# Kernel optimization log

Hardware: AMD Instinct MI355X
Metric: run time of the kernel (lower is better)

The kernel has to match this reference:

```python
import jax, jax.numpy as jnp
import numpy as np

NUM_CAPSULE = 5
DIM_CAPSULE = 5
ROUTINGS = 4
EPS = 1e-7


def squash(t, axis=-1):
    sn = jnp.sum(t * t, axis=axis, keepdims=True)
    scale = sn / (1.0 + sn)
    return scale * t / jnp.sqrt(sn + EPS)


def setup_inputs() -> dict:
    key = jax.random.key(0)
    kx, kw = jax.random.split(key)
    B, I, F = 8192, 256, 80
    x = jax.random.normal(kx, (B, I, F), dtype=jnp.float32)
    # xavier_normal for Linear(80 -> 25): std = sqrt(2/(fan_in+fan_out))
    std = np.sqrt(2.0 / (F + NUM_CAPSULE * DIM_CAPSULE))
    W = jax.random.normal(kw, (NUM_CAPSULE * DIM_CAPSULE, F), dtype=jnp.float32) * std
    return {"x": x, "W": W}


def reference(x, W):
    B, I, _ = x.shape
    # u_hat_vecs: [B, I, N*D] -> [B, N, I, D]
    u_hat = jnp.einsum('bif,of->bio', x, W)
    u_hat = u_hat.reshape(B, I, NUM_CAPSULE, DIM_CAPSULE).transpose(0, 2, 1, 3)
    b = jnp.zeros((B, NUM_CAPSULE, I), dtype=u_hat.dtype)
    outputs = None
    for i in range(ROUTINGS):
        c = jax.nn.softmax(b, axis=1)                         # [B, N, I]
        outputs = squash(jnp.einsum('bni,bnid->bnd', c, u_hat))  # [B, N, D]
        if i < ROUTINGS - 1:
            b = b + jnp.einsum('bnd,bnid->bni', outputs, u_hat)
    return outputs
```

## Files before the change

### kernel.cpp

```cpp
#include <hip/hip_runtime.h>

#define NCAP 5
#define DCAP 5
#define NO 25
#define II 256
#define FF 80
#define NROUT 4
#define EPS 1e-7f
#define USTR 28

typedef _Float16 f16x8 __attribute__((ext_vector_type(8)));
typedef __fp16 fp16x2 __attribute__((ext_vector_type(2)));
typedef float f32x4 __attribute__((ext_vector_type(4)));

__device__ __forceinline__ f16x8 pack8(const float4 a, const float4 c) {
    union { fp16x2 p[4]; f16x8 v; } u;
    u.p[0] = __builtin_amdgcn_cvt_pkrtz(a.x, a.y);
    u.p[1] = __builtin_amdgcn_cvt_pkrtz(a.z, a.w);
    u.p[2] = __builtin_amdgcn_cvt_pkrtz(c.x, c.y);
    u.p[3] = __builtin_amdgcn_cvt_pkrtz(c.z, c.w);
    return u.v;
}

template<int CTRL>
__device__ __forceinline__ float dpp_add(float v) {
    int sw = __builtin_amdgcn_update_dpp(0, __float_as_int(v), CTRL, 0xF, 0xF, true);
    return v + __int_as_float(sw);
}
__device__ __forceinline__ float row16_sum(float v) {
    v = dpp_add<0xB1>(v);
    v = dpp_add<0x4E>(v);
    v = dpp_add<0x141>(v);
    v = dpp_add<0x140>(v);
    return v;
}

__global__ __launch_bounds__(256, 5)
void capsule_mfma(const float* __restrict__ x, const float* __restrict__ W,
                  float* __restrict__ out) {
    const int b    = blockIdx.x;
    const int t    = threadIdx.x;
    const int lane = t & 63;
    const int wv   = t >> 6;
    const int lr   = lane & 15;
    const int lg   = lane >> 4;

    __shared__ __align__(16) float u_lds[II * USTR];
    __shared__ __align__(16) float red[16 * 28];
    __shared__ __align__(16) float fsum[28];

    f16x8 Af[2][3];
#pragma unroll
    for (int ot = 0; ot < 2; ++ot)
#pragma unroll
        for (int ks = 0; ks < 3; ++ks) {
            const int row = ot * 16 + lr;
            const int k0  = ks * 32 + lg * 8;
            if (row < NO && k0 < FF) {
                const float4 a = *reinterpret_cast<const float4*>(&W[row * FF + k0]);
                const float4 c = *reinterpret_cast<const float4*>(&W[row * FF + k0 + 4]);
                Af[ot][ks] = pack8(a, c);
            } else {
                const f16x8 z = {};
                Af[ot][ks] = z;
            }
        }

    const int R0 = wv * 64;
    const float* __restrict__ xbase = x + (size_t)b * II * FF;

#pragma unroll
    for (int nt = 0; nt < 4; ++nt) {
        const int xrow = R0 + nt * 16 + lr;
        const float* __restrict__ xp = xbase + (size_t)xrow * FF;

        f16x8 Bf[3];
#pragma unroll
        for (int ks = 0; ks < 3; ++ks) {
            const int k0 = ks * 32 + lg * 8;
            if (k0 < FF) {
                const float4 a = *reinterpret_cast<const float4*>(xp + k0);
                const float4 c = *reinterpret_cast<const float4*>(xp + k0 + 4);
                Bf[ks] = pack8(a, c);
            } else {
                const f16x8 z = {};
                Bf[ks] = z;
            }
        }

        f32x4 acc0 = {0.f, 0.f, 0.f, 0.f};
        f32x4 acc1 = {0.f, 0.f, 0.f, 0.f};
#pragma unroll
        for (int ks = 0; ks < 3; ++ks) {
            acc0 = __builtin_amdgcn_mfma_f32_16x16x32_f16(Af[0][ks], Bf[ks], acc0, 0, 0, 0);
            acc1 = __builtin_amdgcn_mfma_f32_16x16x32_f16(Af[1][ks], Bf[ks], acc1, 0, 0, 0);
        }

        *reinterpret_cast<float4*>(&u_lds[xrow * USTR + lg * 4]) =
            *reinterpret_cast<float4*>(&acc0);
        if (lg < 3)
            *reinterpret_cast<float4*>(&u_lds[xrow * USTR + 16 + lg * 4]) =
                *reinterpret_cast<float4*>(&acc1);
    }

    float u[NO];
#pragma unroll
    for (int q = 0; q < 6; ++q) {
        const float4 v4 = *reinterpret_cast<const float4*>(&u_lds[t * USTR + q * 4]);
        u[q * 4] = v4.x; u[q * 4 + 1] = v4.y; u[q * 4 + 2] = v4.z; u[q * 4 + 3] = v4.w;
    }
    u[24] = u_lds[t * USTR + 24];

    float bb[NCAP];
#pragma unroll
    for (int n = 0; n < NCAP; ++n) bb[n] = 0.f;

#pragma unroll
    for (int r = 0; r < NROUT; ++r) {
        float c[NCAP];
        if (r == 0) {
#pragma unroll
            for (int n = 0; n < NCAP; ++n) c[n] = 0.2f;
        } else {
            float m = bb[0];
#pragma unroll
            for (int n = 1; n < NCAP; ++n) m = fmaxf(m, bb[n]);
            float ssum = 0.f;
#pragma unroll
            for (int n = 0; n < NCAP; ++n) { c[n] = __expf(bb[n] - m); ssum += c[n]; }
            const float inv = __frcp_rn(ssum);
#pragma unroll
            for (int n = 0; n < NCAP; ++n) c[n] *= inv;
        }

        float p[NO];
#pragma unroll
        for (int o = 0; o < NO; ++o) p[o] = row16_sum(c[o / DCAP] * u[o]);

        if ((t & 15) == 0) {
            float* rg = &red[(t >> 4) * 28];
#pragma unroll
            for (int q = 0; q < 6; ++q)
                *reinterpret_cast<float4*>(&rg[q * 4]) =
                    make_float4(p[q * 4], p[q * 4 + 1], p[q * 4 + 2], p[q * 4 + 3]);
            rg[24] = p[24];
        }
        __syncthreads();

        if (t < NO) {
            float ssum = 0.f;
#pragma unroll
            for (int g = 0; g < 16; ++g) ssum += red[g * 28 + t];
            fsum[t] = ssum;
        }
        __syncthreads();

        if (r < NROUT - 1) {
            float s[NO];
#pragma unroll
            for (int q = 0; q < 6; ++q) {
                const float4 sv = *reinterpret_cast<const float4*>(&fsum[q * 4]);
                s[q * 4 + 0] = sv.x; s[q * 4 + 1] = sv.y;
                s[q * 4 + 2] = sv.z; s[q * 4 + 3] = sv.w;
            }
            s[24] = fsum[24];
#pragma unroll
            for (int n = 0; n < NCAP; ++n) {
                float sn = 0.f, dot = 0.f;
#pragma unroll
                for (int d = 0; d < DCAP; ++d) {
                    const float sv = s[n * DCAP + d];
                    sn  = fmaf(sv, sv, sn);
                    dot = fmaf(sv, u[n * DCAP + d], dot);
                }
                const float scale = sn * __frsqrt_rn(sn + EPS) * __frcp_rn(1.f + sn);
                bb[n] += dot * scale;
            }
        } else {
            if (t < NO) {
                const int n0 = (t / DCAP) * DCAP;
                float sn = 0.f;
#pragma unroll
                for (int d = 0; d < DCAP; ++d) {
                    const float sv = fsum[n0 + d];
                    sn = fmaf(sv, sv, sn);
                }
                const float scale = sn * __frsqrt_rn(sn + EPS) * __frcp_rn(1.f + sn);
                out[(size_t)b * NO + t] = fsum[t] * scale;
            }
        }
    }
}

extern "C" void kernel_launch(void* const* d_in, const int* in_sizes, int n_in,
                              void* d_out, int out_size, void* d_ws, size_t ws_size,
                              hipStream_t stream) {
    const float* x = (const float*)d_in[0];
    const float* W = (const float*)d_in[1];
    float* out = (float*)d_out;
    (void)in_sizes; (void)n_in; (void)out_size; (void)d_ws; (void)ws_size;

    capsule_mfma<<<dim3(8192), dim3(256), 0, stream>>>(x, W, out);
}
```

Measured before the change: 125.5 us.

## Stage x tiles through LDS with double-buffered async global_load_lds

New measurement: 160.0 us. +27.5%, slower.

```diff
diff --git a/kernel.cpp b/kernel.cpp
--- a/kernel.cpp
+++ b/kernel.cpp
@@ -8,10 +8,14 @@
 #define NROUT 4
 #define EPS 1e-7f
 #define USTR 28
+#define CHUNK_F (16 * FF)
 
 typedef _Float16 f16x8 __attribute__((ext_vector_type(8)));
 typedef __fp16 fp16x2 __attribute__((ext_vector_type(2)));
 typedef float f32x4 __attribute__((ext_vector_type(4)));
+
+typedef __attribute__((address_space(1))) const void gvoid;
+typedef __attribute__((address_space(3))) void lvoid;
 
 __device__ __forceinline__ f16x8 pack8(const float4 a, const float4 c) {
     union { fp16x2 p[4]; f16x8 v; } u;
@@ -35,7 +39,7 @@
     return v;
 }
 
-__global__ __launch_bounds__(256, 5)
+__global__ __launch_bounds__(256, 2)
 void capsule_mfma(const float* __restrict__ x, const float* __restrict__ W,
                   float* __restrict__ out) {
     const int b    = blockIdx.x;
@@ -45,6 +49,7 @@
     const int lr   = lane & 15;
     const int lg   = lane >> 4;
 
+    __shared__ __align__(16) float stage[4][2][CHUNK_F];
     __shared__ __align__(16) float u_lds[II * USTR];
     __shared__ __align__(16) float red[16 * 28];
     __shared__ __align__(16) float fsum[28];
@@ -66,21 +71,41 @@
             }
         }
 
-    const int R0 = wv * 64;
-    const float* __restrict__ xbase = x + (size_t)b * II * FF;
+    const float* __restrict__ xw = x + ((size_t)b * II + wv * 64) * FF;
+
+    {
+        float* dst = &stage[wv][0][0];
+#pragma unroll
+        for (int c2 = 0; c2 < 5; ++c2)
+            __builtin_amdgcn_global_load_lds(
+                (gvoid*)(xw + c2 * 256 + lane * 4),
+                (lvoid*)(dst + c2 * 256), 16, 0, 0);
+    }
 
 #pragma unroll
     for (int nt = 0; nt < 4; ++nt) {
-        const int xrow = R0 + nt * 16 + lr;
-        const float* __restrict__ xp = xbase + (size_t)xrow * FF;
+        if (nt < 3) {
+            float* dst = &stage[wv][(nt + 1) & 1][0];
+            const float* src = xw + (nt + 1) * CHUNK_F;
+#pragma unroll
+            for (int c2 = 0; c2 < 5; ++c2)
+                __builtin_amdgcn_global_load_lds(
+                    (gvoid*)(src + c2 * 256 + lane * 4),
+                    (lvoid*)(dst + c2 * 256), 16, 0, 0);
+            asm volatile("s_waitcnt vmcnt(5)" ::: "memory");
+        } else {
+            asm volatile("s_waitcnt vmcnt(0)" ::: "memory");
+        }
+
+        const float* sb = &stage[wv][nt & 1][0];
 
         f16x8 Bf[3];
 #pragma unroll
         for (int ks = 0; ks < 3; ++ks) {
             const int k0 = ks * 32 + lg * 8;
             if (k0 < FF) {
-                const float4 a = *reinterpret_cast<const float4*>(xp + k0);
-                const float4 c = *reinterpret_cast<const float4*>(xp + k0 + 4);
+                const float4 a = *reinterpret_cast<const float4*>(&sb[lr * FF + k0]);
+                const float4 c = *reinterpret_cast<const float4*>(&sb[lr * FF + k0 + 4]);
                 Bf[ks] = pack8(a, c);
             } else {
                 const f16x8 z = {};
@@ -96,6 +121,7 @@
             acc1 = __builtin_amdgcn_mfma_f32_16x16x32_f16(Af[1][ks], Bf[ks], acc1, 0, 0, 0);
         }
 
+        const int xrow = wv * 64 + nt * 16 + lr;
         *reinterpret_cast<float4*>(&u_lds[xrow * USTR + lg * 4]) =
             *reinterpret_cast<float4*>(&acc0);
         if (lg < 3)
```

## Compute routing weighted sums with MFMA over transposed fp16 LDS tiles

Applied to the files above, without the earlier changes.

Result: slower. 179.8 us (+43.3%).

```diff
diff --git a/kernel.cpp b/kernel.cpp
--- a/kernel.cpp
+++ b/kernel.cpp
@@ -7,7 +7,8 @@
 #define FF 80
 #define NROUT 4
 #define EPS 1e-7f
-#define USTR 28
+#define TSTR 260
+#define CSTR 260
 
 typedef _Float16 f16x8 __attribute__((ext_vector_type(8)));
 typedef __fp16 fp16x2 __attribute__((ext_vector_type(2)));
@@ -22,19 +23,6 @@
     return u.v;
 }
 
-template<int CTRL>
-__device__ __forceinline__ float dpp_add(float v) {
-    int sw = __builtin_amdgcn_update_dpp(0, __float_as_int(v), CTRL, 0xF, 0xF, true);
-    return v + __int_as_float(sw);
-}
-__device__ __forceinline__ float row16_sum(float v) {
-    v = dpp_add<0xB1>(v);
-    v = dpp_add<0x4E>(v);
-    v = dpp_add<0x141>(v);
-    v = dpp_add<0x140>(v);
-    return v;
-}
-
 __global__ __launch_bounds__(256, 5)
 void capsule_mfma(const float* __restrict__ x, const float* __restrict__ W,
                   float* __restrict__ out) {
@@ -45,9 +33,9 @@
     const int lr   = lane & 15;
     const int lg   = lane >> 4;
 
-    __shared__ __align__(16) float u_lds[II * USTR];
-    __shared__ __align__(16) float red[16 * 28];
-    __shared__ __align__(16) float fsum[28];
+    __shared__ __align__(16) _Float16 uT[32 * TSTR];
+    __shared__ __align__(16) _Float16 cT[16 * CSTR];
+    __shared__ __align__(16) float s_lds[NCAP][8];
 
     f16x8 Af[2][3];
 #pragma unroll
@@ -66,12 +54,11 @@
             }
         }
 
-    const int R0 = wv * 64;
     const float* __restrict__ xbase = x + (size_t)b * II * FF;
 
 #pragma unroll
     for (int nt = 0; nt < 4; ++nt) {
-        const int xrow = R0 + nt * 16 + lr;
+        const int xrow = wv * 64 + nt * 16 + lr;
         const float* __restrict__ xp = xbase + (size_t)xrow * FF;
 
         f16x8 Bf[3];
@@ -96,20 +83,16 @@
             acc1 = __builtin_amdgcn_mfma_f32_16x16x32_f16(Af[1][ks], Bf[ks], acc1, 0, 0, 0);
         }
 
-        *reinterpret_cast<float4*>(&u_lds[xrow * USTR + lg * 4]) =
-            *reinterpret_cast<float4*>(&acc0);
-        if (lg < 3)
-            *reinterpret_cast<float4*>(&u_lds[xrow * USTR + 16 + lg * 4]) =
-                *reinterpret_cast<float4*>(&acc1);
+#pragma unroll
+        for (int rg = 0; rg < 4; ++rg) {
+            uT[(lg * 4 + rg) * TSTR + xrow]        = (_Float16)acc0[rg];
+            uT[(16 + lg * 4 + rg) * TSTR + xrow]   = (_Float16)acc1[rg];
+        }
     }
 
     float u[NO];
 #pragma unroll
-    for (int q = 0; q < 6; ++q) {
-        const float4 v4 = *reinterpret_cast<const float4*>(&u_lds[t * USTR + q * 4]);
-        u[q * 4] = v4.x; u[q * 4 + 1] = v4.y; u[q * 4 + 2] = v4.z; u[q * 4 + 3] = v4.w;
-    }
-    u[24] = u_lds[t * USTR + 24];
+    for (int o = 0; o < NO; ++o) u[o] = (float)uT[o * TSTR + t];
 
     float bb[NCAP];
 #pragma unroll
@@ -133,43 +116,50 @@
             for (int n = 0; n < NCAP; ++n) c[n] *= inv;
         }
 
-        float p[NO];
 #pragma unroll
-        for (int o = 0; o < NO; ++o) p[o] = row16_sum(c[o / DCAP] * u[o]);
+        for (int n = 0; n < NCAP; ++n) cT[n * CSTR + t] = (_Float16)c[n];
+        __syncthreads();
 
-        if ((t & 15) == 0) {
-            float* rg = &red[(t >> 4) * 28];
+        f32x4 s0 = {0.f, 0.f, 0.f, 0.f};
+        f32x4 s1 = {0.f, 0.f, 0.f, 0.f};
 #pragma unroll
-            for (int q = 0; q < 6; ++q)
-                *reinterpret_cast<float4*>(&rg[q * 4]) =
-                    make_float4(p[q * 4], p[q * 4 + 1], p[q * 4 + 2], p[q * 4 + 3]);
-            rg[24] = p[24];
+        for (int ks = 0; ks < 8; ++ks) {
+            const f16x8 ca = *reinterpret_cast<const f16x8*>(&cT[lr * CSTR + ks * 32 + lg * 8]);
+            const f16x8 u0 = *reinterpret_cast<const f16x8*>(&uT[lr * TSTR + ks * 32 + lg * 8]);
+            const f16x8 u1 = *reinterpret_cast<const f16x8*>(&uT[(16 + lr) * TSTR + ks * 32 + lg * 8]);
+            s0 = __builtin_amdgcn_mfma_f32_16x16x32_f16(ca, u0, s0, 0, 0, 0);
+            s1 = __builtin_amdgcn_mfma_f32_16x16x32_f16(ca, u1, s1, 0, 0, 0);
+        }
+
+        if (wv == 0) {
+            if (lg == 0) {
+                const int n0 = lr / 5;
+                const int d0 = lr - 5 * n0;
+                const float v = (lr < 5) ? s0[0] : (lr < 10) ? s0[1]
+                              : (lr < 15) ? s0[2] : s0[3];
+                s_lds[n0][d0] = v;
+                if (lr < 4) s_lds[3][1 + lr] = s1[3];
+            }
+            if (lg == 1 && lr >= 4 && lr < 9) s_lds[4][lr - 4] = s1[0];
         }
         __syncthreads();
 
-        if (t < NO) {
-            float ssum = 0.f;
+        float sarr[NO];
 #pragma unroll
-            for (int g = 0; g < 16; ++g) ssum += red[g * 28 + t];
-            fsum[t] = ssum;
+        for (int n = 0; n < NCAP; ++n) {
+            const float4 v4 = *reinterpret_cast<const float4*>(&s_lds[n][0]);
+            sarr[n * 5 + 0] = v4.x; sarr[n * 5 + 1] = v4.y;
+            sarr[n * 5 + 2] = v4.z; sarr[n * 5 + 3] = v4.w;
+            sarr[n * 5 + 4] = s_lds[n][4];
         }
-        __syncthreads();
 
         if (r < NROUT - 1) {
-            float s[NO];
-#pragma unroll
-            for (int q = 0; q < 6; ++q) {
-                const float4 sv = *reinterpret_cast<const float4*>(&fsum[q * 4]);
-                s[q * 4 + 0] = sv.x; s[q * 4 + 1] = sv.y;
-                s[q * 4 + 2] = sv.z; s[q * 4 + 3] = sv.w;
-            }
-            s[24] = fsum[24];
 #pragma unroll
             for (int n = 0; n < NCAP; ++n) {
                 float sn = 0.f, dot = 0.f;
 #pragma unroll
                 for (int d = 0; d < DCAP; ++d) {
-                    const float sv = s[n * DCAP + d];
+                    const float sv = sarr[n * DCAP + d];
                     sn  = fmaf(sv, sv, sn);
                     dot = fmaf(sv, u[n * DCAP + d], dot);
                 }
@@ -178,15 +168,15 @@
             }
         } else {
             if (t < NO) {
-                const int n0 = (t / DCAP) * DCAP;
+                const int n0 = t / DCAP;
                 float sn = 0.f;
 #pragma unroll
                 for (int d = 0; d < DCAP; ++d) {
-                    const float sv = fsum[n0 + d];
+                    const float sv = sarr[n0 * DCAP + d];
                     sn = fmaf(sv, sv, sn);
                 }
                 const float scale = sn * __frsqrt_rn(sn + EPS) * __frcp_rn(1.f + sn);
-                out[(size_t)b * NO + t] = fsum[t] * scale;
+                out[(size_t)b * NO + t] = sarr[t] * scale;
             }
         }
     }
```
